# Performance work log

Measured on AMD Instinct MI355X. Metric: run time of the kernel, lower is better.

Reference implementation:

```python
import jax, jax.numpy as jnp
import numpy as np

B, S, F_DIM, FILT = 4096, 41, 128, 128
EPS_BN = 1e-5
EPS_SQ = 1e-21


def squash(v):
    n = jnp.linalg.norm(v, axis=-1, keepdims=True)
    return (1.0 - 1.0 / (jnp.exp(n) + EPS_SQ)) * (v / (n + EPS_SQ))


def position_linear(x, Wstack, bstack, window):
    # x: [B,S,F]; Wstack: [S, window*F, FILT]; bstack: [S, FILT]
    p = window // 2
    Bq, Sq, Fq = x.shape
    xp = jnp.pad(x, ((0, 0), (p, p), (0, 0)))
    idx = jnp.arange(Sq)[:, None] + jnp.arange(window)[None, :]  # [S, window]
    xw = xp[:, idx, :].reshape(Bq, Sq, window * Fq)
    return jax.nn.relu(jnp.einsum('bsf,sfo->bso', xw, Wstack) + bstack[None])


def batchnorm(x, g, b, axes):
    mu = jnp.mean(x, axis=axes, keepdims=True)
    var = jnp.var(x, axis=axes, keepdims=True)
    shape = [1] * x.ndim
    shape[1] = x.shape[1]
    return (x - mu) * jax.lax.rsqrt(var + EPS_BN) * g.reshape(shape) + b.reshape(shape)


def conv1d(x, w, groups=1):
    # x: [N,C,L], w: [O, C//groups, K], padding same (k=3, pad=1)
    return jax.lax.conv_general_dilated(
        x, w, window_strides=(1,), padding=[(1, 1)],
        dimension_numbers=('NCH', 'OIH', 'NCH'), feature_group_count=groups)


def setup_inputs() -> dict:
    key = jax.random.key(0)
    ks = jax.random.split(key, 16)
    sc = lambda fan_in: 1.0 / np.sqrt(fan_in)
    d = {}
    d['x'] = jax.random.randint(ks[0], (B, S), 0, 4, dtype=jnp.int32)
    d['emb'] = jax.random.normal(ks[1], (4, F_DIM), dtype=jnp.float32)
    for i, w in enumerate([3, 5, 7]):
        fin = w * F_DIM
        d[f'W{w}'] = jax.random.uniform(ks[2 + i], (S, fin, FILT), jnp.float32, -sc(fin), sc(fin))
        d[f'b{w}'] = jnp.zeros((S, FILT), jnp.float32)
    d['conv1_w'] = jax.random.uniform(ks[5], (64, 41, 3), jnp.float32, -sc(41 * 3), sc(41 * 3))
    d['conv1_b'] = jnp.zeros((64,), jnp.float32)
    d['bn_g'] = jnp.ones((64,), jnp.float32)
    d['bn_b'] = jnp.zeros((64,), jnp.float32)
    d['caps_w'] = jax.random.uniform(ks[6], (64, 32, 3), jnp.float32, -sc(32 * 3), sc(32 * 3))
    d['caps_b'] = jnp.zeros((64,), jnp.float32)
    d['route_W'] = jax.random.normal(ks[7], (2, 64, F_DIM), jnp.float32)
    d['route_b'] = jnp.zeros((2, 64, 1), jnp.float32)
    d['fc1_w'] = jax.random.uniform(ks[8], (F_DIM, 64), jnp.float32, -sc(F_DIM), sc(F_DIM))
    d['bn1_g'] = jnp.ones((2,), jnp.float32)
    d['bn1_b'] = jnp.zeros((2,), jnp.float32)
    d['fc2_w'] = jax.random.uniform(ks[9], (64, 32), jnp.float32, -sc(64), sc(64))
    d['bn2_g'] = jnp.ones((2,), jnp.float32)
    d['bn2_b'] = jnp.zeros((2,), jnp.float32)
    d['fc3_w'] = jax.random.uniform(ks[10], (32, 1), jnp.float32, -sc(32), sc(32))
    return d


def reference(x, emb, W3, b3, W5, b5, W7, b7, conv1_w, conv1_b, bn_g, bn_b,
              caps_w, caps_b, route_W, route_b,
              fc1_w, bn1_g, bn1_b, fc2_w, bn2_g, bn2_b, fc3_w):
    h = emb[x]                                    # [B,41,128]
    h = position_linear(h, W3, b3, 3)
    h = position_linear(h, W5, b5, 5)
    h = position_linear(h, W7, b7, 7)             # [B,41,128]
    h = conv1d(h, conv1_w) + conv1_b[None, :, None]  # [B,64,128]
    h = jax.nn.relu(batchnorm(h, bn_g, bn_b, axes=(0, 2)))
    h = conv1d(h, caps_w, groups=2) + caps_b[None, :, None]
    h = squash(h)                                 # [B,64,128]
    # Routing layer
    u = h[:, None, :, :] * route_W[None]          # [B,2,64,128]
    c = jnp.sum(u * u, axis=-1, keepdims=True) / jnp.sqrt(128.0)  # [B,2,64,1]
    c = jax.nn.softmax(c, axis=-1)                # softmax over size-1 axis -> ones
    c = c + route_b[None]
    s = squash(jnp.sum(u * c, axis=-2))           # [B,2,128]
    # FC head
    pair = s[:, :, None, :] + s[:, None, :, :]    # [B,2,2,128]
    y = jnp.max(pair, axis=1)                     # [B,2,128]
    y = jax.nn.relu(batchnorm(y @ fc1_w, bn1_g, bn1_b, axes=(0, 2)))
    y = jax.nn.relu(batchnorm(y @ fc2_w, bn2_g, bn2_b, axes=(0, 2)))
    y = jax.nn.sigmoid(y @ fc3_w)                 # [B,2,1]
    return jnp.max(y, axis=1)                     # [B,1]
```

## Files before the change

kernel.cpp:

```cpp
#include <hip/hip_runtime.h>
#include <cstdint>

typedef unsigned short u16;
typedef unsigned int   u32;
typedef __attribute__((ext_vector_type(8))) short bf16x8;
typedef __attribute__((ext_vector_type(4))) float f32x4;

#define DEVFN static __device__ __forceinline__

constexpr int B  = 4096;
constexpr int SQ = 41;

DEVFN float bf2f(u16 v) { return __uint_as_float(((u32)v) << 16); }
DEVFN u16 f2bf(float f) {
  u32 u = __float_as_uint(f);
  u += 0x7fffu + ((u >> 16) & 1u);
  return (u16)(u >> 16);
}
DEVFN u32 pack2(float a, float b) { return (u32)f2bf(a) | ((u32)f2bf(b) << 16); }

DEVFN void gload16(const void* g, void* l) {
  __builtin_amdgcn_global_load_lds(
      (const __attribute__((address_space(1))) unsigned int*)g,
      (__attribute__((address_space(3))) unsigned int*)l, 16, 0, 0);
}

__global__ void k_pack(const float* __restrict__ cw, const float* __restrict__ cpw,
                       const float* __restrict__ rW, const float* __restrict__ rb,
                       u16* __restrict__ wpk, u16* __restrict__ cpk,
                       u16* __restrict__ rwp) {
  int i = blockIdx.x * 256 + threadIdx.x;
  if (i < 12288) {
    int tt = i >> 12, rem = i & 4095, o = rem >> 6, c = rem & 63;
    float v = (c < 41) ? cw[(o * 41 + c) * 3 + tt] : 0.f;
    wpk[(tt * 64 + o) * 64 + (c ^ ((o & 7) << 3))] = f2bf(v);
  } else if (i < 18432) {
    int k = i - 12288;
    int tt = k >> 11, rem = k & 2047, o = rem >> 5, c = rem & 31;
    cpk[(tt * 64 + o) * 32 + (c ^ ((o & 3) << 3))] = f2bf(cpw[(o * 32 + c) * 3 + tt]);
  } else if (i < 34816) {
    int k = i - 18432;
    rwp[k] = f2bf(rW[k] * (1.f + rb[k >> 7]));
  }
}

__global__ void k_combo(const int* __restrict__ x, int* __restrict__ combo) {
  int i = blockIdx.x * 256 + threadIdx.x;
  if (i >= B * SQ) return;
  int b = i / SQ, s = i - b * SQ;
  const int* xb = x + b * SQ;
  int d0 = (s > 0) ? xb[s - 1] : 4;
  int d1 = xb[s];
  int d2 = (s < SQ - 1) ? xb[s + 1] : 4;
  combo[i] = d0 * 25 + d1 * 5 + d2;
}

__global__ void k_gmat(const float* __restrict__ emb, const float* __restrict__ W3,
                       float* __restrict__ G) {
  int s = blockIdx.x / 3, ww = blockIdx.x % 3;
  int o = threadIdx.x;
  const float* Ws = W3 + ((size_t)s * 384 + ww * 128) * 128;
  float a0 = 0.f, a1 = 0.f, a2 = 0.f, a3 = 0.f;
  for (int f = 0; f < 128; ++f) {
    float wg = Ws[(size_t)f * 128 + o];
    a0 = fmaf(emb[f], wg, a0);
    a1 = fmaf(emb[128 + f], wg, a1);
    a2 = fmaf(emb[256 + f], wg, a2);
    a3 = fmaf(emb[384 + f], wg, a3);
  }
  float* Gp = G + ((size_t)(s * 3 + ww) * 5) * 128 + o;
  Gp[0] = a0; Gp[128] = a1; Gp[256] = a2; Gp[384] = a3; Gp[512] = 0.f;
}

__global__ void k_t1(const float* __restrict__ G, const float* __restrict__ b3,
                     float* __restrict__ t1T) {
  int i = blockIdx.x * 256 + threadIdx.x;
  if (i >= SQ * 128 * 125) return;
  int v = i % 125, so = i / 125;
  int s = so >> 7, o = so & 127;
  int d0 = v / 25, r = v % 25;
  int d1 = r / 5, d2 = r % 5;
  float acc = b3[so]
      + G[((size_t)(s * 3 + 0) * 5 + d0) * 128 + o]
      + G[((size_t)(s * 3 + 1) * 5 + d1) * 128 + o]
      + G[((size_t)(s * 3 + 2) * 5 + d2) * 128 + o];
  t1T[i] = fmaxf(acc, 0.f);
}

__global__ __launch_bounds__(128) void k_t2(const float* __restrict__ t1T,
                                            const float* __restrict__ W5,
                                            u16* __restrict__ t2) {
  int bx = blockIdx.x;
  int s = bx / 25; int r = bx % 25;
  int ww = r / 5;  int vt = (r % 5) * 25;
  int o = threadIdx.x;
  int t = s + ww - 2;
  u16* dst = t2 + ((size_t)(s * 5 + ww) * 125 + vt) * 128 + o;
  if (t < 0 || t >= SQ) {
    #pragma unroll
    for (int v = 0; v < 25; ++v) dst[(size_t)v * 128] = 0;
    return;
  }
  float acc[25];
  #pragma unroll
  for (int v = 0; v < 25; ++v) acc[v] = 0.f;
  const float* Ws = W5 + ((size_t)s * 640 + ww * 128) * 128;
  const float* tp = t1T + (size_t)t * 128 * 125 + vt;
  for (int f = 0; f < 128; ++f) {
    float wg = Ws[(size_t)f * 128 + o];
    #pragma unroll
    for (int v = 0; v < 25; ++v) acc[v] = fmaf(tp[f * 125 + v], wg, acc[v]);
  }
  #pragma unroll
  for (int v = 0; v < 25; ++v) dst[(size_t)v * 128] = f2bf(acc[v]);
}

__global__ __launch_bounds__(256) void k_h2(const u16* __restrict__ t2,
                                            const int* __restrict__ combo,
                                            const float* __restrict__ b5,
                                            u16* __restrict__ h2) {
  const int i = blockIdx.x * 256 + threadIdx.x;
  const int o8 = (i & 15) * 8;
  const int rid = i >> 4;
  const int s = rid >> 12, b = rid & 4095;
  float acc[8];
  {
    float4 b0 = *reinterpret_cast<const float4*>(b5 + s * 128 + o8);
    float4 b1 = *reinterpret_cast<const float4*>(b5 + s * 128 + o8 + 4);
    acc[0] = b0.x; acc[1] = b0.y; acc[2] = b0.z; acc[3] = b0.w;
    acc[4] = b1.x; acc[5] = b1.y; acc[6] = b1.z; acc[7] = b1.w;
  }
  const int* cb = combo + b * SQ;
  #pragma unroll
  for (int ww = 0; ww < 5; ++ww) {
    const int t = s + ww - 2;
    if (0 <= t && t < SQ) {
      const int c = cb[t];
      uint4 raw = *reinterpret_cast<const uint4*>(
          t2 + ((size_t)(s * 5 + ww) * 125 + c) * 128 + o8);
      acc[0] += __uint_as_float(raw.x << 16);
      acc[1] += __uint_as_float(raw.x & 0xffff0000u);
      acc[2] += __uint_as_float(raw.y << 16);
      acc[3] += __uint_as_float(raw.y & 0xffff0000u);
      acc[4] += __uint_as_float(raw.z << 16);
      acc[5] += __uint_as_float(raw.z & 0xffff0000u);
      acc[6] += __uint_as_float(raw.w << 16);
      acc[7] += __uint_as_float(raw.w & 0xffff0000u);
    }
  }
  uint4 pk;
  pk.x = pack2(fmaxf(acc[0], 0.f), fmaxf(acc[1], 0.f));
  pk.y = pack2(fmaxf(acc[2], 0.f), fmaxf(acc[3], 0.f));
  pk.z = pack2(fmaxf(acc[4], 0.f), fmaxf(acc[5], 0.f));
  pk.w = pack2(fmaxf(acc[6], 0.f), fmaxf(acc[7], 0.f));
  *reinterpret_cast<uint4*>(h2 + ((size_t)b * SQ + s) * 128 + o8) = pk;
}

__global__ __launch_bounds__(256) void k_w7t(const float* __restrict__ W7,
                                             u16* __restrict__ w7t) {
  __shared__ float tile[64][65];
  const int s = blockIdx.z;
  const int k0 = blockIdx.x * 64;
  const int o0 = blockIdx.y * 64;
  const int t = threadIdx.x;
  #pragma unroll
  for (int i = 0; i < 16; ++i) {
    int idx = t + i * 256;
    int kl = idx >> 6, ol = idx & 63;
    tile[kl][ol] = W7[((size_t)s * 896 + k0 + kl) * 128 + o0 + ol];
  }
  __syncthreads();
  #pragma unroll
  for (int i = 0; i < 16; ++i) {
    int idx = t + i * 256;
    int ol = idx >> 6, kl = idx & 63;
    w7t[((size_t)s * 128 + o0 + ol) * 896 + k0 + kl] = f2bf(tile[kl][ol]);
  }
}

__global__ __launch_bounds__(256) void k_gemm7_mfma(const u16* __restrict__ h2,
                                                    const u16* __restrict__ w7t,
                                                    const float* __restrict__ b7,
                                                    u16* __restrict__ h3) {
  __shared__ u16 As[2][8192];
  __shared__ u16 Bs[2][8192];
  const int s  = blockIdx.y;
  const int b0 = blockIdx.x * 128;
  const int t  = threadIdx.x;
  const int lane = t & 63, w = t >> 6;
  const int wr = w >> 1, wc = w & 1;
  const int lcol = lane & 15, qk = lane >> 4;

  f32x4 acc[4][4];
  #pragma unroll
  for (int i = 0; i < 4; ++i)
    #pragma unroll
    for (int j = 0; j < 4; ++j) acc[i][j] = (f32x4){0.f, 0.f, 0.f, 0.f};

  const u16* wbase = w7t + (size_t)s * 128 * 896;

  auto stage = [&](int kt, int bi) -> int {
    const int k0 = kt * 64;
    const int ww = k0 >> 7, tr = s + ww - 3, kf0 = k0 & 127;
    int issued = 0;
    if (0 <= tr && tr < SQ) {
      #pragma unroll
      for (int it = 0; it < 4; ++it) {
        const int L = it * 4096 + t * 16;
        const int r = L >> 7;
        const int g = (L >> 4) & 7;
        const int gs = g ^ (r & 7);
        gload16(h2 + ((size_t)(b0 + r) * SQ + tr) * 128 + kf0 + gs * 8,
                (char*)As[bi] + it * 4096 + w * 1024);
      }
      issued += 4;
    } else {
      #pragma unroll
      for (int it = 0; it < 4; ++it)
        *reinterpret_cast<uint4*>((char*)As[bi] + it * 4096 + t * 16) =
            make_uint4(0u, 0u, 0u, 0u);
    }
    #pragma unroll
    for (int it = 0; it < 4; ++it) {
      const int L = it * 4096 + t * 16;
      const int o = L >> 7;
      const int g = (L >> 4) & 7;
      const int gs = g ^ (o & 7);
      gload16(wbase + (size_t)o * 896 + k0 + gs * 8,
              (char*)Bs[bi] + it * 4096 + w * 1024);
    }
    return issued + 4;
  };

  stage(0, 0);

  for (int kt = 0; kt < 14; ++kt) {
    const int cur = kt & 1;
    int ni = 0;
    if (kt < 13) ni = stage(kt + 1, cur ^ 1);
    if (ni == 8)      asm volatile("s_waitcnt vmcnt(8) lgkmcnt(0)" ::: "memory");
    else if (ni == 4) asm volatile("s_waitcnt vmcnt(4) lgkmcnt(0)" ::: "memory");
    else              asm volatile("s_waitcnt vmcnt(0) lgkmcnt(0)" ::: "memory");
    __builtin_amdgcn_sched_barrier(0);
    __builtin_amdgcn_s_barrier();
    __builtin_amdgcn_sched_barrier(0);

    const u16* Ac = As[cur];
    const u16* Bc = Bs[cur];
    #pragma unroll
    for (int kk = 0; kk < 2; ++kk) {
      const int gk = kk * 4 + qk;
      bf16x8 av[4], bv[4];
      #pragma unroll
      for (int m = 0; m < 4; ++m) {
        const int zr = wr * 64 + m * 16 + lcol;
        av[m] = *reinterpret_cast<const bf16x8*>(Ac + zr * 64 + ((gk ^ (zr & 7)) << 3));
      }
      #pragma unroll
      for (int n = 0; n < 4; ++n) {
        const int br = wc * 64 + n * 16 + lcol;
        bv[n] = *reinterpret_cast<const bf16x8*>(Bc + br * 64 + ((gk ^ (br & 7)) << 3));
      }
      #pragma unroll
      for (int m = 0; m < 4; ++m)
        #pragma unroll
        for (int n = 0; n < 4; ++n)
          acc[m][n] = __builtin_amdgcn_mfma_f32_16x16x32_bf16(av[m], bv[n], acc[m][n], 0, 0, 0);
    }
    __builtin_amdgcn_sched_barrier(0);
    __builtin_amdgcn_s_barrier();
  }

  const int rq = (lane >> 4) * 4;
  #pragma unroll
  for (int n = 0; n < 4; ++n) {
    const int o = wc * 64 + n * 16 + lcol;
    const float bias = b7[s * 128 + o];
    #pragma unroll
    for (int m = 0; m < 4; ++m) {
      #pragma unroll
      for (int rg = 0; rg < 4; ++rg) {
        const int row = b0 + wr * 64 + m * 16 + rq + rg;
        h3[((size_t)row * SQ + s) * 128 + o] = f2bf(fmaxf(acc[m][n][rg] + bias, 0.f));
      }
    }
  }
}

constexpr int NBC = 8;
__global__ __launch_bounds__(256) void k_conv1(const u16* __restrict__ h3,
                                               const u16* __restrict__ wpk,
                                               const float* __restrict__ cb,
                                               u16* __restrict__ c1T,
                                               float2* __restrict__ part) {
  __shared__ u16 zs[2][6144];
  __shared__ u16 zt[130 * 64];
  __shared__ u16 wl[3 * 64 * 64];
  __shared__ float2 red[4][64];
  const int b0 = blockIdx.x * NBC;
  const int t = threadIdx.x;
  const int lane = t & 63, wv = t >> 6;
  const int r = lane & 15, kq = (lane >> 4) * 8, q = lane >> 4;

  #pragma unroll
  for (int it = 0; it < 6; ++it)
    gload16(wpk + ((size_t)it * 256 + t) * 8, (char*)wl + it * 4096 + wv * 1024);
  #pragma unroll
  for (int it = 0; it < 3; ++it)
    gload16(h3 + (size_t)b0 * (SQ * 128) + ((size_t)it * 256 + t) * 8,
            (char*)zs[0] + it * 4096 + wv * 1024);
  if (t < 64) zt[t] = 0;
  else if (t < 128) zt[129 * 64 + t - 64] = 0;
  __syncthreads();

  for (int i = 0; i < NBC; ++i) {
    const int b = b0 + i;
    const int cur = i & 1;

    {
      const int l = t & 127, jb = (t >> 7) * 32;
      const int sw = ((l + 1) & 7) << 3;
      u16* dst = zt + (l + 1) * 64;
      const u16* srcz = zs[cur];
      #pragma unroll
      for (int j = 0; j < 32; ++j) {
        int c = (jb + j + l) & 63;
        dst[c ^ sw] = (c < 41) ? srcz[c * 128 + l] : (u16)0;
      }
    }
    if (i + 1 < NBC) {
      #pragma unroll
      for (int it = 0; it < 3; ++it)
        gload16(h3 + (size_t)(b + 1) * (SQ * 128) + ((size_t)it * 256 + t) * 8,
                (char*)zs[cur ^ 1] + it * 4096 + wv * 1024);
    }
    asm volatile("s_waitcnt lgkmcnt(0)" ::: "memory");
    __builtin_amdgcn_sched_barrier(0);
    __builtin_amdgcn_s_barrier();
    __builtin_amdgcn_sched_barrier(0);

    f32x4 acc[2][4];
    #pragma unroll
    for (int m = 0; m < 2; ++m)
      #pragma unroll
      for (int n = 0; n < 4; ++n) acc[m][n] = (f32x4){0.f, 0.f, 0.f, 0.f};
    #pragma unroll
    for (int tt = 0; tt < 3; ++tt) {
      #pragma unroll
      for (int kk = 0; kk < 2; ++kk) {
        const int kof = kk * 32 + kq;
        bf16x8 av[2], bv[4];
        #pragma unroll
        for (int m = 0; m < 2; ++m) {
          const int zr = wv * 32 + m * 16 + r + tt;
          av[m] = *reinterpret_cast<const bf16x8*>(zt + zr * 64 + (kof ^ ((zr & 7) << 3)));
        }
        #pragma unroll
        for (int n = 0; n < 4; ++n) {
          const int o = n * 16 + r;
          bv[n] = *reinterpret_cast<const bf16x8*>(wl + (tt * 64 + o) * 64 + (kof ^ ((o & 7) << 3)));
        }
        #pragma unroll
        for (int m = 0; m < 2; ++m)
          #pragma unroll
          for (int n = 0; n < 4; ++n)
            acc[m][n] = __builtin_amdgcn_mfma_f32_16x16x32_bf16(av[m], bv[n], acc[m][n], 0, 0, 0);
      }
    }

    u16* outb = c1T + (size_t)b * 8192;
    #pragma unroll
    for (int n = 0; n < 4; ++n) {
      const int o = n * 16 + r;
      const float bias = cb[o];
      float s1 = 0.f, s2 = 0.f;
      #pragma unroll
      for (int m = 0; m < 2; ++m) {
        #pragma unroll
        for (int rg = 0; rg < 4; ++rg) {
          float v = acc[m][n][rg] + bias;
          s1 += v; s2 += v * v;
          outb[(wv * 32 + m * 16 + q * 4 + rg) * 64 + o] = f2bf(v);
        }
      }
      s1 += __shfl_xor(s1, 16); s1 += __shfl_xor(s1, 32);
      s2 += __shfl_xor(s2, 16); s2 += __shfl_xor(s2, 32);
      if (lane < 16) red[wv][n * 16 + lane] = make_float2(s1, s2);
    }
    __syncthreads();
    if (t < 64) {
      float S = red[0][t].x + red[1][t].x + red[2][t].x + red[3][t].x;
      float Q = red[0][t].y + red[1][t].y + red[2][t].y + red[3][t].y;
      part[(size_t)t * B + b] = make_float2(S, Q);
    }
    __syncthreads();
  }
}

__global__ void k_bnfin(const float2* __restrict__ part, const float* __restrict__ g,
                        const float* __restrict__ bb, float* __restrict__ scale,
                        float* __restrict__ shift) {
  int o = blockIdx.x;
  float s = 0.f, q = 0.f;
  for (int i = threadIdx.x; i < B; i += 256) {
    float2 p = part[(size_t)o * B + i];
    s += p.x; q += p.y;
  }
  #pragma unroll
  for (int off = 32; off; off >>= 1) { s += __shfl_down(s, off); q += __shfl_down(q, off); }
  __shared__ float rs[4], rq[4];
  int wv = threadIdx.x >> 6, ln = threadIdx.x & 63;
  if (ln == 0) { rs[wv] = s; rq[wv] = q; }
  __syncthreads();
  if (threadIdx.x == 0) {
    float S = rs[0] + rs[1] + rs[2] + rs[3];
    float Q = rq[0] + rq[1] + rq[2] + rq[3];
    const float n = (float)B * 128.f;
    float mu = S / n, var = Q / n - mu * mu;
    float sc = g[o] * rsqrtf(var + 1e-5f);
    scale[o] = sc; shift[o] = bb[o] - mu * sc;
  }
}

constexpr int NB = 8;
__global__ __launch_bounds__(256) void k_caps(const u16* __restrict__ c1T,
                                              const float* __restrict__ scale,
                                              const float* __restrict__ shift,
                                              const u16* __restrict__ cpk,
                                              const float* __restrict__ cpb,
                                              const u16* __restrict__ rwp,
                                              const float* __restrict__ f1,
                                              float* __restrict__ y1) {
  __shared__ u16 zt[130 * 64];
  __shared__ u16 wl[3 * 64 * 32];
  __shared__ float f1l[128 * 64];
  __shared__ float red[4][64];
  __shared__ float fl[64];
  __shared__ float sc_s[64], sh_s[64];
  __shared__ float red2[4][2];
  __shared__ float yl[2][128];
  __shared__ float pt[128];
  const int b0 = blockIdx.x * NB;
  const int t = threadIdx.x;
  const int lane = t & 63, wv = t >> 6;
  const int r = lane & 15, kq = (lane >> 4) * 8, q = lane >> 4;

  #pragma unroll
  for (int it = 0; it < 3; ++it)
    gload16(cpk + ((size_t)it * 256 + t) * 8, (char*)wl + it * 4096 + wv * 1024);
  #pragma unroll
  for (int it = 0; it < 8; ++it)
    gload16(f1 + ((size_t)it * 256 + t) * 4, (char*)f1l + it * 4096 + wv * 1024);
  if (t < 64) { sc_s[t] = scale[t]; sh_s[t] = shift[t]; }
  if (t < 64) zt[t] = 0;
  else if (t < 128) zt[129 * 64 + t - 64] = 0;

  uint4 raw[4], rawn[4];
  {
    const u16* src = c1T + (size_t)b0 * 8192;
    #pragma unroll
    for (int p = 0; p < 4; ++p)
      raw[p] = *reinterpret_cast<const uint4*>(src + ((size_t)t + p * 256) * 8);
  }

  for (int i = 0; i < NB; ++i) {
    const int b = b0 + i;
    __syncthreads();

    #pragma unroll
    for (int p = 0; p < 4; ++p) {
      int idx = t + p * 256;
      int l = idx >> 3, c0 = (idx & 7) * 8;
      float vv[8];
      vv[0] = __uint_as_float(raw[p].x << 16); vv[1] = __uint_as_float(raw[p].x & 0xffff0000u);
      vv[2] = __uint_as_float(raw[p].y << 16); vv[3] = __uint_as_float(raw[p].y & 0xffff0000u);
      vv[4] = __uint_as_float(raw[p].z << 16); vv[5] = __uint_as_float(raw[p].z & 0xffff0000u);
      vv[6] = __uint_as_float(raw[p].w << 16); vv[7] = __uint_as_float(raw[p].w & 0xffff0000u);
      float a0 = fmaxf(fmaf(vv[0], sc_s[c0 + 0], sh_s[c0 + 0]), 0.f);
      float a1 = fmaxf(fmaf(vv[1], sc_s[c0 + 1], sh_s[c0 + 1]), 0.f);
      float a2 = fmaxf(fmaf(vv[2], sc_s[c0 + 2], sh_s[c0 + 2]), 0.f);
      float a3 = fmaxf(fmaf(vv[3], sc_s[c0 + 3], sh_s[c0 + 3]), 0.f);
      float a4 = fmaxf(fmaf(vv[4], sc_s[c0 + 4], sh_s[c0 + 4]), 0.f);
      float a5 = fmaxf(fmaf(vv[5], sc_s[c0 + 5], sh_s[c0 + 5]), 0.f);
      float a6 = fmaxf(fmaf(vv[6], sc_s[c0 + 6], sh_s[c0 + 6]), 0.f);
      float a7 = fmaxf(fmaf(vv[7], sc_s[c0 + 7], sh_s[c0 + 7]), 0.f);
      uint4 pk;
      pk.x = pack2(a0, a1); pk.y = pack2(a2, a3);
      pk.z = pack2(a4, a5); pk.w = pack2(a6, a7);
      *reinterpret_cast<uint4*>(zt + (l + 1) * 64 + (c0 ^ (((l + 1) & 7) << 3))) = pk;
    }
    if (i + 1 < NB) {
      const u16* srcn = c1T + (size_t)(b + 1) * 8192;
      #pragma unroll
      for (int p = 0; p < 4; ++p)
        rawn[p] = *reinterpret_cast<const uint4*>(srcn + ((size_t)t + p * 256) * 8);
    }
    __syncthreads();

    f32x4 acc[2][4];
    #pragma unroll
    for (int m = 0; m < 2; ++m)
      #pragma unroll
      for (int n = 0; n < 4; ++n) acc[m][n] = (f32x4){0.f, 0.f, 0.f, 0.f};
    #pragma unroll
    for (int tt = 0; tt < 3; ++tt) {
      bf16x8 av[2][2], bv[4];
      #pragma unroll
      for (int m = 0; m < 2; ++m) {
        const int zr = wv * 32 + m * 16 + r + tt;
        const int sw = (zr & 7) << 3;
        av[m][0] = *reinterpret_cast<const bf16x8*>(zt + zr * 64 + (kq ^ sw));
        av[m][1] = *reinterpret_cast<const bf16x8*>(zt + zr * 64 + ((32 + kq) ^ sw));
      }
      #pragma unroll
      for (int n = 0; n < 4; ++n) {
        const int o = n * 16 + r;
        bv[n] = *reinterpret_cast<const bf16x8*>(wl + (tt * 64 + o) * 32 + (kq ^ ((o & 3) << 3)));
      }
      #pragma unroll
      for (int m = 0; m < 2; ++m)
        #pragma unroll
        for (int n = 0; n < 4; ++n)
          acc[m][n] = __builtin_amdgcn_mfma_f32_16x16x32_bf16(av[m][n >> 1], bv[n], acc[m][n], 0, 0, 0);
    }

    #pragma unroll
    for (int n = 0; n < 4; ++n) {
      const int o = n * 16 + r;
      const float bias = cpb[o];
      float s2 = 0.f;
      #pragma unroll
      for (int m = 0; m < 2; ++m) {
        #pragma unroll
        for (int rg = 0; rg < 4; ++rg) {
          float v = acc[m][n][rg] + bias;
          acc[m][n][rg] = v;
          s2 += v * v;
        }
      }
      s2 += __shfl_xor(s2, 16); s2 += __shfl_xor(s2, 32);
      if (lane < 16) red[wv][n * 16 + lane] = s2;
    }
    __syncthreads();
    if (t < 64) {
      float S = red[0][t] + red[1][t] + red[2][t] + red[3][t];
      float nn = sqrtf(S);
      fl[t] = (1.f - 1.f / (expf(nn) + 1e-21f)) / (nn + 1e-21f);
    }
    __syncthreads();

    float s0[2][4], s1[2][4];
    #pragma unroll
    for (int m = 0; m < 2; ++m)
      #pragma unroll
      for (int rg = 0; rg < 4; ++rg) { s0[m][rg] = 0.f; s1[m][rg] = 0.f; }
    #pragma unroll
    for (int n = 0; n < 4; ++n) {
      const int o = n * 16 + r;
      const float fact = fl[o];
      #pragma unroll
      for (int m = 0; m < 2; ++m) {
        const int l0 = wv * 32 + m * 16 + q * 4;
        uint2 rw0 = *reinterpret_cast<const uint2*>(rwp + (size_t)o * 128 + l0);
        uint2 rw1 = *reinterpret_cast<const uint2*>(rwp + (size_t)(64 + o) * 128 + l0);
        #pragma unroll
        for (int rg = 0; rg < 4; ++rg) {
          float v = acc[m][n][rg] * fact;
          u32 w0w = (rg < 2) ? rw0.x : rw0.y;
          u32 w1w = (rg < 2) ? rw1.x : rw1.y;
          float w0 = __uint_as_float((rg & 1) ? (w0w & 0xffff0000u) : (w0w << 16));
          float w1 = __uint_as_float((rg & 1) ? (w1w & 0xffff0000u) : (w1w << 16));
          s0[m][rg] = fmaf(v, w0, s0[m][rg]);
          s1[m][rg] = fmaf(v, w1, s1[m][rg]);
        }
      }
    }
    #pragma unroll
    for (int m = 0; m < 2; ++m)
      #pragma unroll
      for (int rg = 0; rg < 4; ++rg) {
        #pragma unroll
        for (int off = 1; off <= 8; off <<= 1) {
          s0[m][rg] += __shfl_xor(s0[m][rg], off);
          s1[m][rg] += __shfl_xor(s1[m][rg], off);
        }
      }
    float n0 = 0.f, n1 = 0.f;
    #pragma unroll
    for (int m = 0; m < 2; ++m)
      #pragma unroll
      for (int rg = 0; rg < 4; ++rg) {
        n0 = fmaf(s0[m][rg], s0[m][rg], n0);
        n1 = fmaf(s1[m][rg], s1[m][rg], n1);
      }
    n0 += __shfl_xor(n0, 16); n0 += __shfl_xor(n0, 32);
    n1 += __shfl_xor(n1, 16); n1 += __shfl_xor(n1, 32);
    if (lane == 0) { red2[wv][0] = n0; red2[wv][1] = n1; }
    __syncthreads();
    {
      float t0 = red2[0][0] + red2[1][0] + red2[2][0] + red2[3][0];
      float t1 = red2[0][1] + red2[1][1] + red2[2][1] + red2[3][1];
      float nn0 = sqrtf(t0), nn1 = sqrtf(t1);
      float fa0 = (1.f - 1.f / (expf(nn0) + 1e-21f)) / (nn0 + 1e-21f);
      float fa1 = (1.f - 1.f / (expf(nn1) + 1e-21f)) / (nn1 + 1e-21f);
      if (r == 0) {
        #pragma unroll
        for (int m = 0; m < 2; ++m)
          #pragma unroll
          for (int rg = 0; rg < 4; ++rg) {
            float v0 = s0[m][rg] * fa0, v1 = s1[m][rg] * fa1;
            float mx = fmaxf(v0, v1);
            int l = wv * 32 + m * 16 + q * 4 + rg;
            yl[0][l] = v0 + mx;
            yl[1][l] = v1 + mx;
          }
      }
    }
    __syncthreads();

    {
      const int h = t >> 7, idx = t & 127;
      const int jj = idx >> 6, qq = idx & 63;
      float a = 0.f;
      const float* yrow = &yl[jj][h * 64];
      const float* frow = f1l + (h * 64) * 64 + qq;
      #pragma unroll 8
      for (int tt = 0; tt < 64; ++tt)
        a = fmaf(yrow[tt], frow[tt * 64], a);
      if (h == 1) pt[idx] = a;
      __syncthreads();
      if (h == 0)
        y1[((size_t)b * 2 + jj) * 64 + qq] = a + pt[idx];
    }

    #pragma unroll
    for (int p = 0; p < 4; ++p) raw[p] = rawn[p];
  }
}

__global__ __launch_bounds__(256) void k_bnstat_part(const float* __restrict__ y,
                                                     float2* __restrict__ pp,
                                                     int perShift) {
  const int jj = blockIdx.y;
  const int per = 1 << perShift;
  const int n4 = (B << perShift) >> 2;
  const int p4shift = perShift - 2;
  const int p4mask = (per >> 2) - 1;
  float s = 0.f, q = 0.f;
  for (int i = blockIdx.x * 256 + threadIdx.x; i < n4; i += 64 * 256) {
    int bI = i >> p4shift, c4 = (i & p4mask) * 4;
    float4 v = *reinterpret_cast<const float4*>(
        y + (size_t)bI * (per * 2) + jj * per + c4);
    s += v.x + v.y + v.z + v.w;
    q += v.x * v.x + v.y * v.y + v.z * v.z + v.w * v.w;
  }
  #pragma unroll
  for (int off = 32; off; off >>= 1) { s += __shfl_down(s, off); q += __shfl_down(q, off); }
  __shared__ float rs[4], rq[4];
  int wv = threadIdx.x >> 6, ln = threadIdx.x & 63;
  if (ln == 0) { rs[wv] = s; rq[wv] = q; }
  __syncthreads();
  if (threadIdx.x == 0)
    pp[jj * 64 + blockIdx.x] =
        make_float2(rs[0] + rs[1] + rs[2] + rs[3], rq[0] + rq[1] + rq[2] + rq[3]);
}

__global__ void k_bnstat_fin(const float2* __restrict__ pp, const float* __restrict__ g,
                             const float* __restrict__ bb, float* __restrict__ scale,
                             float* __restrict__ shift, int perShift) {
  const int jj = blockIdx.x;
  float2 p = pp[jj * 64 + threadIdx.x];
  float s = p.x, q = p.y;
  #pragma unroll
  for (int off = 32; off; off >>= 1) { s += __shfl_down(s, off); q += __shfl_down(q, off); }
  if (threadIdx.x == 0) {
    float fn = (float)(B << perShift);
    float mu = s / fn, var = q / fn - mu * mu;
    float sc = g[jj] * rsqrtf(var + 1e-5f);
    scale[jj] = sc; shift[jj] = bb[jj] - mu * sc;
  }
}

__global__ void k_fc2(const float* __restrict__ y1, const float* __restrict__ sc1,
                      const float* __restrict__ sh1, const float* __restrict__ f2,
                      float* __restrict__ y2) {
  int t = threadIdx.x;
  int b = blockIdx.x * 4 + (t >> 6);
  int jj = (t >> 5) & 1, r = t & 31;
  float sc = sc1[jj], sh = sh1[jj];
  const float* yb = y1 + (size_t)b * 128 + jj * 64;
  float acc = 0.f;
  for (int q = 0; q < 64; ++q) {
    float v = fmaxf(fmaf(yb[q], sc, sh), 0.f);
    acc = fmaf(v, f2[q * 32 + r], acc);
  }
  y2[(size_t)b * 64 + jj * 32 + r] = acc;
}

__global__ void k_head(const float* __restrict__ y2, const float* __restrict__ sc2,
                       const float* __restrict__ sh2, const float* __restrict__ f3,
                       float* __restrict__ out) {
  int b = blockIdx.x * 256 + threadIdx.x;
  if (b >= B) return;
  const float* yb = y2 + (size_t)b * 64;
  float c0 = sc2[0], d0 = sh2[0], c1v = sc2[1], d1 = sh2[1];
  float a0 = 0.f, a1 = 0.f;
  for (int r = 0; r < 32; ++r) {
    float w = f3[r];
    a0 = fmaf(fmaxf(fmaf(yb[r], c0, d0), 0.f), w, a0);
    a1 = fmaf(fmaxf(fmaf(yb[32 + r], c1v, d1), 0.f), w, a1);
  }
  float s0 = 1.f / (1.f + expf(-a0));
  float s1 = 1.f / (1.f + expf(-a1));
  out[b] = fmaxf(s0, s1);
}

constexpr size_t SZ_H2    = (size_t)B * SQ * 128 * 2;
constexpr size_t SZ_C1    = (size_t)B * 64 * 128 * 2;
constexpr size_t OFF_H2   = 0;
constexpr size_t OFF_H3   = SZ_H2;
constexpr size_t R1       = 2 * SZ_H2;
constexpr size_t OFF_G    = R1;
constexpr size_t OFF_T1   = OFF_G + 314880;
constexpr size_t OFF_T2   = OFF_T1 + 2624000;
constexpr size_t OFF_CMB  = OFF_T2 + 6560000;
constexpr size_t OFF_W7T  = OFF_CMB + 671744;
constexpr size_t OFF_C1   = R1;
constexpr size_t R2       = R1 + SZ_C1;
constexpr size_t OFF_PART = R2;
constexpr size_t OFF_Y1   = OFF_PART + 2097152;
constexpr size_t OFF_Y2   = OFF_Y1 + 2097152;
constexpr size_t OFF_SM   = OFF_Y2 + 1048576;
constexpr size_t OFF_BNP  = OFF_SM + 1024;
constexpr size_t OFF_WPK  = OFF_BNP + 1024;
constexpr size_t OFF_CPK  = OFF_WPK + 24576;
constexpr size_t OFF_RWP  = OFF_CPK + 12288;

extern "C" void kernel_launch(void* const* d_in, const int* in_sizes, int n_in,
                              void* d_out, int out_size, void* d_ws, size_t ws_size,
                              hipStream_t stream) {
  const int*   x   = (const int*)d_in[0];
  const float* emb = (const float*)d_in[1];
  const float* W3  = (const float*)d_in[2];
  const float* b3  = (const float*)d_in[3];
  const float* W5  = (const float*)d_in[4];
  const float* b5  = (const float*)d_in[5];
  const float* W7  = (const float*)d_in[6];
  const float* b7  = (const float*)d_in[7];
  const float* c1w = (const float*)d_in[8];
  const float* c1b = (const float*)d_in[9];
  const float* bng = (const float*)d_in[10];
  const float* bnb = (const float*)d_in[11];
  const float* cpw = (const float*)d_in[12];
  const float* cpb = (const float*)d_in[13];
  const float* rW  = (const float*)d_in[14];
  const float* rb  = (const float*)d_in[15];
  const float* f1  = (const float*)d_in[16];
  const float* g1  = (const float*)d_in[17];
  const float* bb1 = (const float*)d_in[18];
  const float* f2  = (const float*)d_in[19];
  const float* g2  = (const float*)d_in[20];
  const float* bb2 = (const float*)d_in[21];
  const float* f3  = (const float*)d_in[22];

  char* wsb = (char*)d_ws;
  u16*    h2p   = (u16*)(wsb + OFF_H2);
  u16*    h3p   = (u16*)(wsb + OFF_H3);
  float*  Gp    = (float*)(wsb + OFF_G);
  float*  t1p   = (float*)(wsb + OFF_T1);
  u16*    t2p   = (u16*)(wsb + OFF_T2);
  int*    cmbp  = (int*)(wsb + OFF_CMB);
  u16*    w7tp  = (u16*)(wsb + OFF_W7T);
  u16*    c1p   = (u16*)(wsb + OFF_C1);
  float2* partp = (float2*)(wsb + OFF_PART);
  float*  y1p   = (float*)(wsb + OFF_Y1);
  float*  y2p   = (float*)(wsb + OFF_Y2);
  float*  scp   = (float*)(wsb + OFF_SM);
  float*  shp   = scp + 64;
  float*  sc1p  = shp + 64;
  float*  sh1p  = sc1p + 2;
  float*  sc2p  = sh1p + 2;
  float*  sh2p  = sc2p + 2;
  float2* bnpp  = (float2*)(wsb + OFF_BNP);
  u16*    wpkp  = (u16*)(wsb + OFF_WPK);
  u16*    cpkp  = (u16*)(wsb + OFF_CPK);
  u16*    rwpp  = (u16*)(wsb + OFF_RWP);

  k_pack<<<136, 256, 0, stream>>>(c1w, cpw, rW, rb, wpkp, cpkp, rwpp);
  k_combo<<<(B * SQ + 255) / 256, 256, 0, stream>>>(x, cmbp);
  k_w7t<<<dim3(14, 2, SQ), 256, 0, stream>>>(W7, w7tp);
  k_gmat<<<SQ * 3, 128, 0, stream>>>(emb, W3, Gp);
  k_t1<<<(SQ * 128 * 125 + 255) / 256, 256, 0, stream>>>(Gp, b3, t1p);
  k_t2<<<SQ * 25, 128, 0, stream>>>(t1p, W5, t2p);
  k_h2<<<(B * SQ * 16) / 256, 256, 0, stream>>>(t2p, cmbp, b5, h2p);
  k_gemm7_mfma<<<dim3(32, SQ), 256, 0, stream>>>(h2p, w7tp, b7, h3p);
  k_conv1<<<B / NBC, 256, 0, stream>>>(h3p, wpkp, c1b, c1p, partp);
  k_bnfin<<<64, 256, 0, stream>>>(partp, bng, bnb, scp, shp);
  k_caps<<<B / NB, 256, 0, stream>>>(c1p, scp, shp, cpkp, cpb, rwpp, f1, y1p);
  k_bnstat_part<<<dim3(64, 2), 256, 0, stream>>>(y1p, bnpp, 6);
  k_bnstat_fin<<<2, 64, 0, stream>>>(bnpp, g1, bb1, sc1p, sh1p, 6);
  k_fc2<<<B / 4, 256, 0, stream>>>(y1p, sc1p, sh1p, f2, y2p);
  k_bnstat_part<<<dim3(64, 2), 256, 0, stream>>>(y2p, bnpp, 5);
  k_bnstat_fin<<<2, 64, 0, stream>>>(bnpp, g2, bb2, sc2p, sh2p, 5);
  k_head<<<B / 256, 256, 0, stream>>>(y2p, sc2p, sh2p, f3, (float*)d_out);
}
```

Before: 236.0 us.

## Move t2 window-5 stage to bf16 MFMA and fuse BN statistics into producers

Replaces the scalar fp32 k_t2 loop with a bf16 MFMA GEMM per (position, window offset). It uses a new transposed bf16 copy of W5 and a padded bf16 t1 table with swizzled LDS tiles. Separately, the FC-head batchnorm partial sums are now accumulated inside k_caps and k_fc2, which removes two k_bnstat_part passes over y1/y2. This lowers precision of the t1/W5 products to bf16, and the W5 transpose buffer reuses the h2 region, which is safe only because it is consumed before h2 is written.

```diff
diff --git a/kernel.cpp b/kernel.cpp
--- a/kernel.cpp
+++ b/kernel.cpp
@@ -73,46 +73,121 @@
 }
 
 __global__ void k_t1(const float* __restrict__ G, const float* __restrict__ b3,
-                     float* __restrict__ t1T) {
+                     u16* __restrict__ t1b) {
   int i = blockIdx.x * 256 + threadIdx.x;
-  if (i >= SQ * 128 * 125) return;
-  int v = i % 125, so = i / 125;
-  int s = so >> 7, o = so & 127;
-  int d0 = v / 25, r = v % 25;
-  int d1 = r / 5, d2 = r % 5;
-  float acc = b3[so]
-      + G[((size_t)(s * 3 + 0) * 5 + d0) * 128 + o]
-      + G[((size_t)(s * 3 + 1) * 5 + d1) * 128 + o]
-      + G[((size_t)(s * 3 + 2) * 5 + d2) * 128 + o];
-  t1T[i] = fmaxf(acc, 0.f);
-}
-
-__global__ __launch_bounds__(128) void k_t2(const float* __restrict__ t1T,
-                                            const float* __restrict__ W5,
-                                            u16* __restrict__ t2) {
-  int bx = blockIdx.x;
-  int s = bx / 25; int r = bx % 25;
-  int ww = r / 5;  int vt = (r % 5) * 25;
-  int o = threadIdx.x;
-  int t = s + ww - 2;
-  u16* dst = t2 + ((size_t)(s * 5 + ww) * 125 + vt) * 128 + o;
-  if (t < 0 || t >= SQ) {
-    #pragma unroll
-    for (int v = 0; v < 25; ++v) dst[(size_t)v * 128] = 0;
-    return;
-  }
-  float acc[25];
-  #pragma unroll
-  for (int v = 0; v < 25; ++v) acc[v] = 0.f;
-  const float* Ws = W5 + ((size_t)s * 640 + ww * 128) * 128;
-  const float* tp = t1T + (size_t)t * 128 * 125 + vt;
-  for (int f = 0; f < 128; ++f) {
-    float wg = Ws[(size_t)f * 128 + o];
-    #pragma unroll
-    for (int v = 0; v < 25; ++v) acc[v] = fmaf(tp[f * 125 + v], wg, acc[v]);
-  }
-  #pragma unroll
-  for (int v = 0; v < 25; ++v) dst[(size_t)v * 128] = f2bf(acc[v]);
+  int f = i & 127, v = (i >> 7) & 127, s = i >> 14;
+  u16 out = 0;
+  if (v < 125) {
+    int d0 = v / 25, r = v % 25;
+    int d1 = r / 5, d2 = r % 5;
+    float acc = b3[s * 128 + f]
+        + G[((size_t)(s * 3 + 0) * 5 + d0) * 128 + f]
+        + G[((size_t)(s * 3 + 1) * 5 + d1) * 128 + f]
+        + G[((size_t)(s * 3 + 2) * 5 + d2) * 128 + f];
+    out = f2bf(fmaxf(acc, 0.f));
+  }
+  t1b[i] = out;
+}
+
+__global__ __launch_bounds__(256) void k_w5t(const float* __restrict__ W5,
+                                             u16* __restrict__ w5t) {
+  __shared__ float tile[64][65];
+  const int sw = blockIdx.z;
+  const int s = sw / 5, w = sw % 5;
+  const int f0 = blockIdx.x * 64;
+  const int o0 = blockIdx.y * 64;
+  const int t = threadIdx.x;
+  const float* Ws = W5 + ((size_t)s * 640 + w * 128) * 128;
+  #pragma unroll
+  for (int i = 0; i < 16; ++i) {
+    int idx = t + i * 256;
+    int fl = idx >> 6, ol = idx & 63;
+    tile[fl][ol] = Ws[(size_t)(f0 + fl) * 128 + o0 + ol];
+  }
+  __syncthreads();
+  #pragma unroll
+  for (int i = 0; i < 16; ++i) {
+    int idx = t + i * 256;
+    int ol = idx >> 6, fl = idx & 63;
+    w5t[((size_t)sw * 128 + o0 + ol) * 128 + f0 + fl] = f2bf(tile[fl][ol]);
+  }
+}
+
+__global__ __launch_bounds__(256) void k_t2_mfma(const u16* __restrict__ t1b,
+                                                 const u16* __restrict__ w5t,
+                                                 u16* __restrict__ t2) {
+  __shared__ u16 As[2][8192];
+  __shared__ u16 Bs[2][8192];
+  const int sw = blockIdx.x;
+  const int s = sw / 5, w5 = sw % 5;
+  const int tw = s + w5 - 2;
+  if (tw < 0 || tw >= SQ) return;
+  const int t = threadIdx.x;
+  const int lane = t & 63, w = t >> 6;
+  const int wr = w >> 1, wc = w & 1;
+  const int lcol = lane & 15, qk = lane >> 4;
+
+  const u16* abase = t1b + (size_t)tw * 128 * 128;
+  const u16* bbase = w5t + (size_t)sw * 128 * 128;
+  #pragma unroll
+  for (int h = 0; h < 2; ++h) {
+    #pragma unroll
+    for (int it = 0; it < 4; ++it) {
+      const int L = it * 4096 + t * 16;
+      const int r = L >> 7, g = (L >> 4) & 7;
+      const int gs = g ^ (r & 7);
+      gload16(abase + (size_t)r * 128 + h * 64 + gs * 8,
+              (char*)As[h] + it * 4096 + w * 1024);
+      gload16(bbase + (size_t)r * 128 + h * 64 + gs * 8,
+              (char*)Bs[h] + it * 4096 + w * 1024);
+    }
+  }
+  __syncthreads();
+
+  f32x4 acc[4][4];
+  #pragma unroll
+  for (int i = 0; i < 4; ++i)
+    #pragma unroll
+    for (int j = 0; j < 4; ++j) acc[i][j] = (f32x4){0.f, 0.f, 0.f, 0.f};
+
+  #pragma unroll
+  for (int h = 0; h < 2; ++h) {
+    #pragma unroll
+    for (int kk = 0; kk < 2; ++kk) {
+      const int gk = kk * 4 + qk;
+      bf16x8 av[4], bv[4];
+      #pragma unroll
+      for (int m = 0; m < 4; ++m) {
+        const int zr = wr * 64 + m * 16 + lcol;
+        av[m] = *reinterpret_cast<const bf16x8*>(&As[h][zr * 64 + ((gk ^ (zr & 7)) << 3)]);
+      }
+      #pragma unroll
+      for (int n = 0; n < 4; ++n) {
+        const int br = wc * 64 + n * 16 + lcol;
+        bv[n] = *reinterpret_cast<const bf16x8*>(&Bs[h][br * 64 + ((gk ^ (br & 7)) << 3)]);
+      }
+      #pragma unroll
+      for (int m = 0; m < 4; ++m)
+        #pragma unroll
+        for (int n = 0; n < 4; ++n)
+          acc[m][n] = __builtin_amdgcn_mfma_f32_16x16x32_bf16(av[m], bv[n], acc[m][n], 0, 0, 0);
+    }
+  }
+
+  u16* dst = t2 + (size_t)sw * 125 * 128;
+  const int rq = (lane >> 4) * 4;
+  #pragma unroll
+  for (int n = 0; n < 4; ++n) {
+    const int o = wc * 64 + n * 16 + lcol;
+    #pragma unroll
+    for (int m = 0; m < 4; ++m) {
+      #pragma unroll
+      for (int rg = 0; rg < 4; ++rg) {
+        const int row = wr * 64 + m * 16 + rq + rg;
+        if (row < 125) dst[(size_t)row * 128 + o] = f2bf(acc[m][n][rg]);
+      }
+    }
+  }
 }
 
 __global__ __launch_bounds__(256) void k_h2(const u16* __restrict__ t2,
@@ -430,7 +505,8 @@
                                               const float* __restrict__ cpb,
                                               const u16* __restrict__ rwp,
                                               const float* __restrict__ f1,
-                                              float* __restrict__ y1) {
+                                              float* __restrict__ y1,
+                                              float2* __restrict__ ppy1) {
   __shared__ u16 zt[130 * 64];
   __shared__ u16 wl[3 * 64 * 32];
   __shared__ float f1l[128 * 64];
@@ -444,6 +520,7 @@
   const int t = threadIdx.x;
   const int lane = t & 63, wv = t >> 6;
   const int r = lane & 15, kq = (lane >> 4) * 8, q = lane >> 4;
+  float ysum = 0.f, ysq = 0.f;
 
   #pragma unroll
   for (int it = 0; it < 3; ++it)
@@ -629,30 +706,40 @@
         a = fmaf(yrow[tt], frow[tt * 64], a);
       if (h == 1) pt[idx] = a;
       __syncthreads();
-      if (h == 0)
-        y1[((size_t)b * 2 + jj) * 64 + qq] = a + pt[idx];
+      float val = 0.f;
+      if (h == 0) {
+        val = a + pt[idx];
+        y1[((size_t)b * 2 + jj) * 64 + qq] = val;
+      }
+      ysum += val; ysq += val * val;
     }
 
     #pragma unroll
     for (int p = 0; p < 4; ++p) raw[p] = rawn[p];
   }
-}
-
-__global__ __launch_bounds__(256) void k_bnstat_part(const float* __restrict__ y,
-                                                     float2* __restrict__ pp,
-                                                     int perShift) {
-  const int jj = blockIdx.y;
-  const int per = 1 << perShift;
-  const int n4 = (B << perShift) >> 2;
-  const int p4shift = perShift - 2;
-  const int p4mask = (per >> 2) - 1;
+
+  #pragma unroll
+  for (int off = 32; off; off >>= 1) {
+    ysum += __shfl_down(ysum, off);
+    ysq  += __shfl_down(ysq, off);
+  }
+  __syncthreads();
+  if (lane == 0) { red2[wv][0] = ysum; red2[wv][1] = ysq; }
+  __syncthreads();
+  if (t == 0) ppy1[blockIdx.x] = make_float2(red2[0][0] + red2[2][0],
+                                             red2[0][1] + red2[2][1]);
+  if (t == 1) ppy1[512 + blockIdx.x] = make_float2(red2[1][0] + red2[3][0],
+                                                   red2[1][1] + red2[3][1]);
+}
+
+__global__ void k_bnstat_fin(const float2* __restrict__ pp, const float* __restrict__ g,
+                             const float* __restrict__ bb, float* __restrict__ scale,
+                             float* __restrict__ shift, int perShift, int nparts) {
+  const int jj = blockIdx.x;
   float s = 0.f, q = 0.f;
-  for (int i = blockIdx.x * 256 + threadIdx.x; i < n4; i += 64 * 256) {
-    int bI = i >> p4shift, c4 = (i & p4mask) * 4;
-    float4 v = *reinterpret_cast<const float4*>(
-        y + (size_t)bI * (per * 2) + jj * per + c4);
-    s += v.x + v.y + v.z + v.w;
-    q += v.x * v.x + v.y * v.y + v.z * v.z + v.w * v.w;
+  for (int i = threadIdx.x; i < nparts; i += 256) {
+    float2 p = pp[jj * nparts + i];
+    s += p.x; q += p.y;
   }
   #pragma unroll
   for (int off = 32; off; off >>= 1) { s += __shfl_down(s, off); q += __shfl_down(q, off); }
@@ -660,22 +747,11 @@
   int wv = threadIdx.x >> 6, ln = threadIdx.x & 63;
   if (ln == 0) { rs[wv] = s; rq[wv] = q; }
   __syncthreads();
-  if (threadIdx.x == 0)
-    pp[jj * 64 + blockIdx.x] =
-        make_float2(rs[0] + rs[1] + rs[2] + rs[3], rq[0] + rq[1] + rq[2] + rq[3]);
-}
-
-__global__ void k_bnstat_fin(const float2* __restrict__ pp, const float* __restrict__ g,
-                             const float* __restrict__ bb, float* __restrict__ scale,
-                             float* __restrict__ shift, int perShift) {
-  const int jj = blockIdx.x;
-  float2 p = pp[jj * 64 + threadIdx.x];
-  float s = p.x, q = p.y;
-  #pragma unroll
-  for (int off = 32; off; off >>= 1) { s += __shfl_down(s, off); q += __shfl_down(q, off); }
   if (threadIdx.x == 0) {
+    float S = rs[0] + rs[1] + rs[2] + rs[3];
+    float Q = rq[0] + rq[1] + rq[2] + rq[3];
     float fn = (float)(B << perShift);
-    float mu = s / fn, var = q / fn - mu * mu;
+    float mu = S / fn, var = Q / fn - mu * mu;
     float sc = g[jj] * rsqrtf(var + 1e-5f);
     scale[jj] = sc; shift[jj] = bb[jj] - mu * sc;
   }
@@ -683,7 +759,8 @@
 
 __global__ void k_fc2(const float* __restrict__ y1, const float* __restrict__ sc1,
                       const float* __restrict__ sh1, const float* __restrict__ f2,
-                      float* __restrict__ y2) {
+                      float* __restrict__ y2, float2* __restrict__ ppy2) {
+  __shared__ float2 r2[8];
   int t = threadIdx.x;
   int b = blockIdx.x * 4 + (t >> 6);
   int jj = (t >> 5) & 1, r = t & 31;
@@ -695,6 +772,17 @@
     acc = fmaf(v, f2[q * 32 + r], acc);
   }
   y2[(size_t)b * 64 + jj * 32 + r] = acc;
+  float s = acc, q2 = acc * acc;
+  #pragma unroll
+  for (int off = 16; off; off >>= 1) { s += __shfl_down(s, off); q2 += __shfl_down(q2, off); }
+  if ((t & 31) == 0) r2[t >> 5] = make_float2(s, q2);
+  __syncthreads();
+  if (t == 0) ppy2[blockIdx.x] =
+      make_float2(r2[0].x + r2[2].x + r2[4].x + r2[6].x,
+                  r2[0].y + r2[2].y + r2[4].y + r2[6].y);
+  if (t == 1) ppy2[1024 + blockIdx.x] =
+      make_float2(r2[1].x + r2[3].x + r2[5].x + r2[7].x,
+                  r2[1].y + r2[3].y + r2[5].y + r2[7].y);
 }
 
 __global__ void k_head(const float* __restrict__ y2, const float* __restrict__ sc2,
@@ -718,6 +806,7 @@
 constexpr size_t SZ_H2    = (size_t)B * SQ * 128 * 2;
 constexpr size_t SZ_C1    = (size_t)B * 64 * 128 * 2;
 constexpr size_t OFF_H2   = 0;
+constexpr size_t OFF_W5T  = 0;
 constexpr size_t OFF_H3   = SZ_H2;
 constexpr size_t R1       = 2 * SZ_H2;
 constexpr size_t OFF_G    = R1;
@@ -731,8 +820,7 @@
 constexpr size_t OFF_Y1   = OFF_PART + 2097152;
 constexpr size_t OFF_Y2   = OFF_Y1 + 2097152;
 constexpr size_t OFF_SM   = OFF_Y2 + 1048576;
-constexpr size_t OFF_BNP  = OFF_SM + 1024;
-constexpr size_t OFF_WPK  = OFF_BNP + 1024;
+constexpr size_t OFF_WPK  = OFF_SM + 1024;
 constexpr size_t OFF_CPK  = OFF_WPK + 24576;
 constexpr size_t OFF_RWP  = OFF_CPK + 12288;
 
@@ -765,14 +853,17 @@
 
   char* wsb = (char*)d_ws;
   u16*    h2p   = (u16*)(wsb + OFF_H2);
+  u16*    w5tp  = (u16*)(wsb + OFF_W5T);
   u16*    h3p   = (u16*)(wsb + OFF_H3);
   float*  Gp    = (float*)(wsb + OFF_G);
-  float*  t1p   = (float*)(wsb + OFF_T1);
+  u16*    t1p   = (u16*)(wsb + OFF_T1);
   u16*    t2p   = (u16*)(wsb + OFF_T2);
   int*    cmbp  = (int*)(wsb + OFF_CMB);
   u16*    w7tp  = (u16*)(wsb + OFF_W7T);
   u16*    c1p   = (u16*)(wsb + OFF_C1);
   float2* partp = (float2*)(wsb + OFF_PART);
+  float2* ppy1  = partp;
+  float2* ppy2  = partp + 2048;
   float*  y1p   = (float*)(wsb + OFF_Y1);
   float*  y2p   = (float*)(wsb + OFF_Y2);
   float*  scp   = (float*)(wsb + OFF_SM);
@@ -781,26 +872,24 @@
   float*  sh1p  = sc1p + 2;
   float*  sc2p  = sh1p + 2;
   float*  sh2p  = sc2p + 2;
-  float2* bnpp  = (float2*)(wsb + OFF_BNP);
   u16*    wpkp  = (u16*)(wsb + OFF_WPK);
   u16*    cpkp  = (u16*)(wsb + OFF_CPK);
   u16*    rwpp  = (u16*)(wsb + OFF_RWP);
 
   k_pack<<<136, 256, 0, stream>>>(c1w, cpw, rW, rb, wpkp, cpkp, rwpp);
   k_combo<<<(B * SQ + 255) / 256, 256, 0, stream>>>(x, cmbp);
+  k_w5t<<<dim3(2, 2, SQ * 5), 256, 0, stream>>>(W5, w5tp);
   k_w7t<<<dim3(14, 2, SQ), 256, 0, stream>>>(W7, w7tp);
   k_gmat<<<SQ * 3, 128, 0, stream>>>(emb, W3, Gp);
-  k_t1<<<(SQ * 128 * 125 + 255) / 256, 256, 0, stream>>>(Gp, b3, t1p);
-  k_t2<<<SQ * 25, 128, 0, stream>>>(t1p, W5, t2p);
+  k_t1<<<SQ * 128 * 128 / 256, 256, 0, stream>>>(Gp, b3, t1p);
+  k_t2_mfma<<<SQ * 5, 256, 0, stream>>>(t1p, w5tp, t2p);
   k_h2<<<(B * SQ * 16) / 256, 256, 0, stream>>>(t2p, cmbp, b5, h2p);
   k_gemm7_mfma<<<dim3(32, SQ), 256, 0, stream>>>(h2p, w7tp, b7, h3p);
   k_conv1<<<B / NBC, 256, 0, stream>>>(h3p, wpkp, c1b, c1p, partp);
   k_bnfin<<<64, 256, 0, stream>>>(partp, bng, bnb, scp, shp);
-  k_caps<<<B / NB, 256, 0, stream>>>(c1p, scp, shp, cpkp, cpb, rwpp, f1, y1p);
-  k_bnstat_part<<<dim3(64, 2), 256, 0, stream>>>(y1p, bnpp, 6);
-  k_bnstat_fin<<<2, 64, 0, stream>>>(bnpp, g1, bb1, sc1p, sh1p, 6);
-  k_fc2<<<B / 4, 256, 0, stream>>>(y1p, sc1p, sh1p, f2, y2p);
-  k_bnstat_part<<<dim3(64, 2), 256, 0, stream>>>(y2p, bnpp, 5);
-  k_bnstat_fin<<<2, 64, 0, stream>>>(bnpp, g2, bb2, sc2p, sh2p, 5);
+  k_caps<<<B / NB, 256, 0, stream>>>(c1p, scp, shp, cpkp, cpb, rwpp, f1, y1p, ppy1);
+  k_bnstat_fin<<<2, 256, 0, stream>>>(ppy1, g1, bb1, sc1p, sh1p, 6, 512);
+  k_fc2<<<B / 4, 256, 0, stream>>>(y1p, sc1p, sh1p, f2, y2p, ppy2);
+  k_bnstat_fin<<<2, 256, 0, stream>>>(ppy2, g2, bb2, sc2p, sh2p, 5, 1024);
   k_head<<<B / 256, 256, 0, stream>>>(y2p, sc2p, sh2p, f3, (float*)d_out);
 }
```

New measurement: 216.3 us. 8.3% less time.
